# Optimization experiments

Hardware: AMD Instinct MI355X
Metric: run time of the kernel (lower is better)

## Reference

```python
import jax, jax.numpy as jnp
import numpy as np
import math

N_HIDDEN = 256
N_BLOCKS = 15
N_BINARY = 8
NODE_DIM = 16
EDGE_DIM = 4
N_NODES = 20000
N_EDGES = 100000


def setup_inputs() -> dict:
    key = jax.random.key(0)
    ks = iter(jax.random.split(key, 64))

    def lin(i, o):
        return (jax.random.normal(next(ks), (i, o), jnp.float32) / np.sqrt(i)).astype(jnp.float32)

    def lin_s(i, o):  # stacked over N_BLOCKS layers
        return (jax.random.normal(next(ks), (N_BLOCKS, i, o), jnp.float32) / np.sqrt(i)).astype(jnp.float32)

    inp = {
        "x": jax.random.uniform(next(ks), (N_NODES, NODE_DIM), jnp.float32),
        "edge_index": jax.random.randint(next(ks), (2, N_EDGES), 0, N_NODES, jnp.int32),
        "edge_attr": jax.random.uniform(next(ks), (N_EDGES, EDGE_DIM), jnp.float32),
        # conv1: in = NODE_DIM
        "Wq1": lin(NODE_DIM, N_HIDDEN), "bq1": jnp.zeros((N_HIDDEN,), jnp.float32),
        "Wk1": lin(NODE_DIM, N_HIDDEN), "bk1": jnp.zeros((N_HIDDEN,), jnp.float32),
        "Wv1": lin(NODE_DIM, N_HIDDEN), "bv1": jnp.zeros((N_HIDDEN,), jnp.float32),
        "We1": lin(EDGE_DIM, N_HIDDEN),  # lin_edge has no bias in PyG TransformerConv
        "Ws1": lin(NODE_DIM, N_HIDDEN), "bs1": jnp.zeros((N_HIDDEN,), jnp.float32),
        # 15 residual blocks: in = N_HIDDEN, stacked params
        "Wq": lin_s(N_HIDDEN, N_HIDDEN), "bq": jnp.zeros((N_BLOCKS, N_HIDDEN), jnp.float32),
        "Wk": lin_s(N_HIDDEN, N_HIDDEN), "bk": jnp.zeros((N_BLOCKS, N_HIDDEN), jnp.float32),
        "Wv": lin_s(N_HIDDEN, N_HIDDEN), "bv": jnp.zeros((N_BLOCKS, N_HIDDEN), jnp.float32),
        "We": lin_s(EDGE_DIM, N_HIDDEN),
        "Ws": lin_s(N_HIDDEN, N_HIDDEN), "bs": jnp.zeros((N_BLOCKS, N_HIDDEN), jnp.float32),
        # output head
        "Wl": lin(N_HIDDEN, N_BINARY), "bl": jnp.zeros((N_BINARY,), jnp.float32),
        "scale": jnp.asarray([2.0 ** i for i in range(N_BINARY)], jnp.float32),
    }
    return inp


def _tconv(h, ea_emb_src_params, src, dst, n):
    """PyG TransformerConv (heads=1) with edge features."""
    wq, bq, wk, bk, wv, bv, we, ws, bs, ea = ea_emb_src_params
    q = h @ wq + bq          # [N, C]
    k = h @ wk + bk
    v = h @ wv + bv
    e = ea @ we              # [E, C] edge embedding
    ke = k[src] + e          # [E, C]
    alpha = jnp.sum(q[dst] * ke, axis=-1) / math.sqrt(N_HIDDEN)  # [E]
    m = jax.ops.segment_max(alpha, dst, num_segments=n)
    a = jnp.exp(alpha - m[dst])
    s = jax.ops.segment_sum(a, dst, num_segments=n)
    attn = a / (s[dst] + 1e-16)
    out = jax.ops.segment_sum(attn[:, None] * (v[src] + e), dst, num_segments=n)
    return out + h @ ws + bs  # root_weight skip


def reference(x, edge_index, edge_attr,
              Wq1, bq1, Wk1, bk1, Wv1, bv1, We1, Ws1, bs1,
              Wq, bq, Wk, bk, Wv, bv, We, Ws, bs,
              Wl, bl, scale):
    n = x.shape[0]
    src, dst = edge_index[0], edge_index[1]
    h = jnp.log(x + 1.0)
    ea = jnp.log(edge_attr + 1.0)
    h = _tconv(h, (Wq1, bq1, Wk1, bk1, Wv1, bv1, We1, Ws1, bs1, ea), src, dst, n)

    def block(carry, p):
        wq, bq_, wk, bk_, wv, bv_, we, ws, bs_ = p
        std = jax.lax.stop_gradient(jnp.std(carry, axis=-1, ddof=1, keepdims=True))
        h2 = jax.nn.relu(carry / std)
        y = _tconv(h2, (wq, bq_, wk, bk_, wv, bv_, we, ws, bs_, ea), src, dst, n)
        return carry + y, None

    h, _ = jax.lax.scan(block, h, (Wq, bq, Wk, bk, Wv, bv, We, Ws, bs))
    h = h / math.sqrt(N_BLOCKS)
    h = h @ Wl + bl
    return jnp.sum(h * scale, axis=-1, keepdims=True)
```

## Files before the change

kernel.cpp:

```cpp
#include <hip/hip_runtime.h>
#include <math.h>

typedef short bf16x8 __attribute__((ext_vector_type(8)));
typedef float f32x4 __attribute__((ext_vector_type(4)));
typedef _Float16 h16x8 __attribute__((ext_vector_type(8)));
typedef _Float16 h16x4 __attribute__((ext_vector_type(4)));
typedef _Float16 h16x2 __attribute__((ext_vector_type(2)));

static __device__ __forceinline__ float wred_sum(float v){
  #pragma unroll
  for (int o = 32; o > 0; o >>= 1) v += __shfl_xor(v, o, 64);
  return v;
}

static __device__ __forceinline__ unsigned short f2bf(float x){
  union { float f; unsigned int u; } c; c.f = x;
  unsigned int u = c.u;
  return (unsigned short)((u + 0x7FFFu + ((u >> 16) & 1u)) >> 16);
}

__global__ void prep_kernel(const float* __restrict__ x, const float* __restrict__ ea_in,
                            float* __restrict__ hx, float* __restrict__ ea,
                            int nx, int ne){
  int i = blockIdx.x * 256 + threadIdx.x;
  if (i < nx) hx[i] = logf(x[i] + 1.f);
  if (i < ne) ea[i] = logf(ea_in[i] + 1.f);
}

__global__ void zero_kernel(int* __restrict__ c, int n){
  int i = blockIdx.x * 256 + threadIdx.x;
  if (i < n) c[i] = 0;
}

__global__ void hist_kernel(const int* __restrict__ dst, int* __restrict__ counts, int E){
  int i = blockIdx.x * 256 + threadIdx.x;
  if (i < E) atomicAdd(&counts[dst[i]], 1);
}

__global__ __launch_bounds__(1024) void scan_kernel(const int* __restrict__ counts,
                                                    int* __restrict__ row_ptr,
                                                    int* __restrict__ cursor, int N){
  __shared__ int woff[16];
  __shared__ int carry_s;
  int t = threadIdx.x, lane = t & 63, wid = t >> 6;
  if (t == 0) carry_s = 0;
  __syncthreads();
  for (int base = 0; base < N; base += 1024){
    int i = base + t;
    int v = (i < N) ? counts[i] : 0;
    int incl = v;
    #pragma unroll
    for (int o = 1; o < 64; o <<= 1){
      int tmp = __shfl_up(incl, o, 64);
      if (lane >= o) incl += tmp;
    }
    if (lane == 63) woff[wid] = incl;
    __syncthreads();
    if (t < 16){
      int w = woff[t];
      int inc2 = w;
      #pragma unroll
      for (int o = 1; o < 16; o <<= 1){
        int tmp = __shfl_up(inc2, o, 16);
        if (t >= o) inc2 += tmp;
      }
      woff[t] = inc2 - w;
    }
    __syncthreads();
    int ex = carry_s + woff[wid] + incl - v;
    if (i < N){ row_ptr[i] = ex; cursor[i] = ex; }
    __syncthreads();
    if (t == 1023) carry_s = ex + v;
    __syncthreads();
  }
  if (t == 0) row_ptr[N] = carry_s;
}

__global__ void scatter_kernel(const int* __restrict__ src, const int* __restrict__ dst,
                               const float* __restrict__ ea,
                               int* __restrict__ cursor,
                               int* __restrict__ src_csr, float* __restrict__ ea_csr, int E){
  int i = blockIdx.x * 256 + threadIdx.x;
  if (i < E){
    int p = atomicAdd(&cursor[dst[i]], 1);
    src_csr[p] = src[i];
    *(float4*)&ea_csr[(size_t)p * 4] = *(const float4*)&ea[(size_t)i * 4];
  }
}

__global__ void wlscale_kernel(const float* __restrict__ Wl, const float* __restrict__ bl,
                               const float* __restrict__ scale, float* __restrict__ wlsc){
  int c = threadIdx.x;
  float s = 0.f;
  #pragma unroll
  for (int j = 0; j < 8; j++) s += Wl[c * 8 + j] * scale[j];
  wlsc[c] = s;
  if (c == 0){
    float b = 0.f;
    #pragma unroll
    for (int j = 0; j < 8; j++) b += bl[j] * scale[j];
    wlsc[256] = b;
  }
}

__global__ __launch_bounds__(256) void pack_w_kernel(
    const float* __restrict__ Wq, const float* __restrict__ Wk,
    const float* __restrict__ Wv, const float* __restrict__ Ws,
    unsigned short* __restrict__ Wp)
{
  __shared__ float t[32][33];
  int l   = blockIdx.z;
  int k0  = blockIdx.x * 32;
  int n0g = blockIdx.y * 32;
  int w   = n0g >> 8;
  int n0  = n0g & 255;
  const float* W = ((w == 0) ? Wq : (w == 1) ? Wk : (w == 2) ? Wv : Ws) + (size_t)l * 65536;
  int rr = threadIdx.x >> 3;
  int cc = (threadIdx.x & 7) * 4;
  float4 vv = *(const float4*)&W[(size_t)(k0 + rr) * 256 + n0 + cc];
  t[rr][cc + 0] = vv.x; t[rr][cc + 1] = vv.y; t[rr][cc + 2] = vv.z; t[rr][cc + 3] = vv.w;
  __syncthreads();
  ushort4 o;
  o.x = f2bf(t[cc + 0][rr]);
  o.y = f2bf(t[cc + 1][rr]);
  o.z = f2bf(t[cc + 2][rr]);
  o.w = f2bf(t[cc + 3][rr]);
  *(ushort4*)&Wp[(size_t)l * 262144 + (size_t)(n0g + rr) * 256 + k0 + cc] = o;
}

__global__ void pack_b_kernel(const float* __restrict__ bq, const float* __restrict__ bk,
                              const float* __restrict__ bv, const float* __restrict__ bs,
                              float* __restrict__ bp){
  int i = blockIdx.x * 256 + threadIdx.x;
  if (i < 15 * 256){
    int l = i >> 8, n = i & 255;
    bp[l * 1024 + 0   + n] = bq[i];
    bp[l * 1024 + 256 + n] = bk[i];
    bp[l * 1024 + 512 + n] = bv[i];
    bp[l * 1024 + 768 + n] = bs[i];
  }
}

__global__ __launch_bounds__(256) void pack_wqe_kernel(
    const float* __restrict__ Wq, const float* __restrict__ We,
    const float* __restrict__ bq, float* __restrict__ Wqe, float* __restrict__ bqe)
{
  __shared__ float We_s[1024];
  int l = blockIdx.x;
  for (int i = threadIdx.x; i < 1024; i += 256) We_s[i] = We[(size_t)l * 1024 + i];
  __syncthreads();
  int k = threadIdx.x;
  const float* wrow = Wq + (size_t)l * 65536 + (size_t)k * 256;
  float s0 = 0.f, s1 = 0.f, s2 = 0.f, s3 = 0.f;
  for (int c = 0; c < 256; c++){
    float wv = wrow[c];
    s0 += wv * We_s[c];
    s1 += wv * We_s[256 + c];
    s2 += wv * We_s[512 + c];
    s3 += wv * We_s[768 + c];
  }
  float4 o; o.x = s0; o.y = s1; o.z = s2; o.w = s3;
  *(float4*)&Wqe[((size_t)l * 256 + k) * 4] = o;
  if (k < 4){
    float b = 0.f;
    for (int c = 0; c < 256; c++) b += bq[l * 256 + c] * We_s[k * 256 + c];
    bqe[l * 4 + k] = b;
  }
}

__global__ __launch_bounds__(256) void qwe1_kernel(const _Float16* __restrict__ qkvh,
                                                   const float* __restrict__ We1,
                                                   float* __restrict__ qwe, int N){
  __shared__ float We_s[1024];
  for (int i = threadIdx.x; i < 1024; i += 256) We_s[i] = We1[i];
  __syncthreads();
  int wid = threadIdx.x >> 6, lane = threadIdx.x & 63;
  int n = blockIdx.x * 4 + wid;
  if (n >= N) return;
  int c0 = lane * 4;
  h16x4 qr = *(const h16x4*)&qkvh[(size_t)n * 768 + c0];
  float q0 = (float)qr[0], q1 = (float)qr[1], q2 = (float)qr[2], q3 = (float)qr[3];
  float4 o;
  #pragma unroll
  for (int j = 0; j < 4; j++){
    float s = q0 * We_s[j * 256 + c0] + q1 * We_s[j * 256 + c0 + 1]
            + q2 * We_s[j * 256 + c0 + 2] + q3 * We_s[j * 256 + c0 + 3];
    s = wred_sum(s);
    if (j == 0) o.x = s; else if (j == 1) o.y = s; else if (j == 2) o.z = s; else o.w = s;
  }
  if (lane == 0) *(float4*)&qwe[(size_t)n * 4] = o;
}

__global__ __launch_bounds__(256) void gemm1_kernel(
    const float* __restrict__ A,
    const float* __restrict__ W0, const float* __restrict__ W1,
    const float* __restrict__ W2, const float* __restrict__ W3,
    const float* __restrict__ B0, const float* __restrict__ B1,
    const float* __restrict__ B2, const float* __restrict__ B3,
    _Float16* __restrict__ qkvh, _Float16* __restrict__ slh, int N)
{
  __shared__ float As[64][16];
  int nb = blockIdx.x * 64;
  {
    int row = nb + (threadIdx.x >> 2);
    int qq = (threadIdx.x & 3) * 4;
    float4 a = make_float4(0.f, 0.f, 0.f, 0.f);
    if (row < N) a = *(const float4*)&A[row * 16 + qq];
    *(float4*)&As[threadIdx.x >> 2][qq] = a;
  }
  __syncthreads();
  int col = threadIdx.x;
  #pragma unroll
  for (int w = 0; w < 4; w++){
    const float* W  = (w == 0) ? W0 : (w == 1) ? W1 : (w == 2) ? W2 : W3;
    const float* Bi = (w == 0) ? B0 : (w == 1) ? B1 : (w == 2) ? B2 : B3;
    float wr[16];
    #pragma unroll
    for (int kk = 0; kk < 16; kk++) wr[kk] = W[kk * 256 + col];
    float bias = Bi[col];
    for (int r = 0; r < 64; r++){
      int row = nb + r;
      if (row >= N) break;
      float acc = bias;
      #pragma unroll
      for (int kk = 0; kk < 16; kk++) acc += As[r][kk] * wr[kk];
      if (w < 3) qkvh[(size_t)row * 768 + w * 256 + col] = (_Float16)acc;
      else       slh[(size_t)row * 256 + col] = (_Float16)acc;
    }
  }
}

__global__ __launch_bounds__(256, 3) void gemm_mfma_kernel(
    const unsigned short* __restrict__ A,
    const unsigned short* __restrict__ Wp,
    const float* __restrict__ bp,
    _Float16* __restrict__ qkvh,
    _Float16* __restrict__ slh,
    int M)
{
  __shared__ unsigned short lds[2 * 128 * 64];
  unsigned short* ldsA = lds;
  unsigned short* ldsB = lds + 128 * 64;
  const int tid  = threadIdx.x;
  const int wave = tid >> 6, lane = tid & 63;
  const int wm = wave >> 1, wn = wave & 1;
  const int rt  = (int)gridDim.x;
  const int lin = (int)blockIdx.x + rt * (int)blockIdx.y;
  const int gt  = (lin & 7) * rt + (lin >> 3);
  const int m0 = (gt >> 3) * 128;
  const int n0 = (gt & 7) * 128;

  f32x4 acc[4][4] = {};

  const int srow  = lane >> 3;
  const int sc16  = lane & 7;
  const int skgrp = sc16 ^ (srow & 7);

  for (int k0 = 0; k0 < 256; k0 += 64){
    #pragma unroll
    for (int it = 0; it < 4; ++it){
      int lrow = wave * 32 + it * 8;
      const unsigned short* gA = A + (size_t)(m0 + lrow + srow) * 256 + k0 + skgrp * 8;
      __builtin_amdgcn_global_load_lds((const __attribute__((address_space(1))) unsigned int*)gA,
          (__attribute__((address_space(3))) unsigned int*)(ldsA + lrow * 64), 16, 0, 0);
      const unsigned short* gB = Wp + (size_t)(n0 + lrow + srow) * 256 + k0 + skgrp * 8;
      __builtin_amdgcn_global_load_lds((const __attribute__((address_space(1))) unsigned int*)gB,
          (__attribute__((address_space(3))) unsigned int*)(ldsB + lrow * 64), 16, 0, 0);
    }
    __syncthreads();

    bf16x8 af[4][2], bfr[4][2];
    #pragma unroll
    for (int mb = 0; mb < 4; ++mb){
      int r = wm * 64 + mb * 16 + (lane & 15);
      #pragma unroll
      for (int ks = 0; ks < 2; ++ks){
        int kg = ks * 4 + (lane >> 4);
        af[mb][ks] = *(const bf16x8*)&ldsA[r * 64 + ((kg ^ (r & 7)) * 8)];
      }
    }
    #pragma unroll
    for (int nb = 0; nb < 4; ++nb){
      int r = wn * 64 + nb * 16 + (lane & 15);
      #pragma unroll
      for (int ks = 0; ks < 2; ++ks){
        int kg = ks * 4 + (lane >> 4);
        bfr[nb][ks] = *(const bf16x8*)&ldsB[r * 64 + ((kg ^ (r & 7)) * 8)];
      }
    }
    #pragma unroll
    for (int mb = 0; mb < 4; ++mb){
      #pragma unroll
      for (int nb = 0; nb < 4; ++nb){
        acc[mb][nb] = __builtin_amdgcn_mfma_f32_16x16x32_bf16(af[mb][0], bfr[nb][0], acc[mb][nb], 0, 0, 0);
        acc[mb][nb] = __builtin_amdgcn_mfma_f32_16x16x32_bf16(af[mb][1], bfr[nb][1], acc[mb][nb], 0, 0, 0);
      }
    }
    __syncthreads();
  }

  #pragma unroll
  for (int nb = 0; nb < 4; ++nb){
    int col = n0 + wn * 64 + nb * 16 + (lane & 15);
    float bias = bp[col];
    #pragma unroll
    for (int mb = 0; mb < 4; ++mb){
      #pragma unroll
      for (int r4 = 0; r4 < 4; ++r4){
        int row = m0 + wm * 64 + mb * 16 + (lane >> 4) * 4 + r4;
        if (row < M){
          float o = acc[mb][nb][r4] + bias;
          if (col < 768) qkvh[(size_t)row * 768 + col] = (_Float16)o;
          else           slh[(size_t)row * 256 + (col - 768)] = (_Float16)o;
        }
      }
    }
  }
}

__global__ __launch_bounds__(256) void agg_kernel(
    const _Float16* __restrict__ qkvh,
    const _Float16* __restrict__ slh,
    const float* __restrict__ qwe,
    const float* __restrict__ ea_csr,
    const int* __restrict__ src_csr,
    const float* __restrict__ We,
    const float* __restrict__ Wqe_next,
    const float* __restrict__ bqe_next,
    const int* __restrict__ row_ptr,
    const float* __restrict__ h_in, float* __restrict__ h_out,
    unsigned short* __restrict__ h2b, float* __restrict__ qwe_out,
    const float* __restrict__ wlsc, float* __restrict__ out,
    int RESID, int LAST, int N)
{
  int wid = threadIdx.x >> 6, lane = threadIdx.x & 63;
  int n = blockIdx.x * 4 + wid;
  if (n >= N) return;
  int c0 = lane * 4;
  int glane = lane >> 3;
  int slane = lane & 7;

  float4 qwe4 = *(const float4*)&qwe[(size_t)n * 4];
  const _Float16* qrow = qkvh + (size_t)n * 768 + slane * 32;
  union hu { h16x8 v; h16x2 p[4]; };
  hu qf[4];
  #pragma unroll
  for (int u = 0; u < 4; ++u) qf[u].v = *(const h16x8*)(qrow + u * 8);

  float m = -INFINITY, ssum = 0.f;
  float a0 = 0.f, a1 = 0.f, a2 = 0.f, a3 = 0.f;
  float ec0 = 0.f, ec1 = 0.f, ec2 = 0.f, ec3 = 0.f;
  int e0 = row_ptr[n], e1 = row_ptr[n + 1];

  for (int base = e0; base < e1; base += 8){
    int cnt = min(8, e1 - base);
    int eg = base + ((glane < cnt) ? glane : (cnt - 1));
    int sg = src_csr[eg];
    float4 eag = *(const float4*)&ea_csr[(size_t)eg * 4];
    const _Float16* krow = qkvh + (size_t)sg * 768 + 256 + slane * 32;
    float dot = 0.f;
    #pragma unroll
    for (int u = 0; u < 4; ++u){
      hu kf;
      kf.v = *(const h16x8*)(krow + u * 8);
      #pragma unroll
      for (int pp = 0; pp < 4; ++pp){
#if __has_builtin(__builtin_amdgcn_fdot2)
        dot = __builtin_amdgcn_fdot2(qf[u].p[pp], kf.p[pp], dot, false);
#else
        dot += (float)qf[u].p[pp][0] * (float)kf.p[pp][0] + (float)qf[u].p[pp][1] * (float)kf.p[pp][1];
#endif
      }
    }
    #pragma unroll
    for (int o = 1; o < 8; o <<= 1) dot += __shfl_xor(dot, o, 64);
    float alpha_g = (dot + qwe4.x * eag.x + qwe4.y * eag.y + qwe4.z * eag.z + qwe4.w * eag.w) * 0.0625f;
    float aj[8];
    #pragma unroll
    for (int j = 0; j < 8; ++j){
      aj[j] = __shfl(alpha_g, j << 3, 64);
      if (j >= cnt) aj[j] = -INFINITY;
    }
    float mc = fmaxf(fmaxf(fmaxf(aj[0], aj[1]), fmaxf(aj[2], aj[3])),
                     fmaxf(fmaxf(aj[4], aj[5]), fmaxf(aj[6], aj[7])));
    float mn = fmaxf(m, mc);
    float corr = expf(m - mn);
    float wj[8];
    float wtot = 0.f;
    #pragma unroll
    for (int j = 0; j < 8; ++j){
      wj[j] = (j < cnt) ? expf(aj[j] - mn) : 0.f;
      wtot += wj[j];
    }
    ssum = ssum * corr + wtot;
    a0 *= corr; a1 *= corr; a2 *= corr; a3 *= corr;
    ec0 *= corr; ec1 *= corr; ec2 *= corr; ec3 *= corr;
    m = mn;
    #pragma unroll
    for (int j = 0; j < 8; ++j){
      if (j < cnt){
        int sj = __shfl(sg, j << 3, 64);
        h16x4 vr = *(const h16x4*)&qkvh[(size_t)sj * 768 + 512 + c0];
        float4 er = *(const float4*)&ea_csr[(size_t)(base + j) * 4];
        a0 += wj[j] * (float)vr[0];
        a1 += wj[j] * (float)vr[1];
        a2 += wj[j] * (float)vr[2];
        a3 += wj[j] * (float)vr[3];
        ec0 += wj[j] * er.x;
        ec1 += wj[j] * er.y;
        ec2 += wj[j] * er.z;
        ec3 += wj[j] * er.w;
      }
    }
  }

  float inv = 1.f / (ssum + 1e-16f);
  float4 W0 = *(const float4*)&We[0 * 256 + c0];
  float4 W1 = *(const float4*)&We[1 * 256 + c0];
  float4 W2 = *(const float4*)&We[2 * 256 + c0];
  float4 W3 = *(const float4*)&We[3 * 256 + c0];
  float emb0 = ec0 * W0.x + ec1 * W1.x + ec2 * W2.x + ec3 * W3.x;
  float emb1 = ec0 * W0.y + ec1 * W1.y + ec2 * W2.y + ec3 * W3.y;
  float emb2 = ec0 * W0.z + ec1 * W1.z + ec2 * W2.z + ec3 * W3.z;
  float emb3 = ec0 * W0.w + ec1 * W1.w + ec2 * W2.w + ec3 * W3.w;
  h16x4 slv4 = *(const h16x4*)&slh[(size_t)n * 256 + c0];
  float y0 = (a0 + emb0) * inv + (float)slv4[0];
  float y1 = (a1 + emb1) * inv + (float)slv4[1];
  float y2 = (a2 + emb2) * inv + (float)slv4[2];
  float y3 = (a3 + emb3) * inv + (float)slv4[3];
  float o0, o1, o2, o3;
  if (RESID){
    float4 hp = *(const float4*)&h_in[(size_t)n * 256 + c0];
    o0 = hp.x + y0; o1 = hp.y + y1; o2 = hp.z + y2; o3 = hp.w + y3;
  } else {
    o0 = y0; o1 = y1; o2 = y2; o3 = y3;
  }
  if (LAST){
    float4 wv = *(const float4*)&wlsc[c0];
    float pp = o0 * wv.x + o1 * wv.y + o2 * wv.z + o3 * wv.w;
    pp = wred_sum(pp);
    if (lane == 0) out[n] = pp * (1.f / sqrtf(15.f)) + wlsc[256];
    return;
  }
  float4 ho; ho.x = o0; ho.y = o1; ho.z = o2; ho.w = o3;
  *(float4*)&h_out[(size_t)n * 256 + c0] = ho;
  float mean = wred_sum(o0 + o1 + o2 + o3) * (1.f / 256.f);
  float d0 = o0 - mean, d1 = o1 - mean, d2 = o2 - mean, d3 = o3 - mean;
  float var = wred_sum(d0 * d0 + d1 * d1 + d2 * d2 + d3 * d3) * (1.f / 255.f);
  float invstd = 1.f / sqrtf(var);
  float t0 = fmaxf(o0 * invstd, 0.f);
  float t1 = fmaxf(o1 * invstd, 0.f);
  float t2 = fmaxf(o2 * invstd, 0.f);
  float t3 = fmaxf(o3 * invstd, 0.f);
  ushort4 hb;
  hb.x = f2bf(t0); hb.y = f2bf(t1); hb.z = f2bf(t2); hb.w = f2bf(t3);
  *(ushort4*)&h2b[(size_t)n * 256 + c0] = hb;
  if (Wqe_next){
    float4 g0 = *(const float4*)&Wqe_next[(c0 + 0) * 4];
    float4 g1 = *(const float4*)&Wqe_next[(c0 + 1) * 4];
    float4 g2 = *(const float4*)&Wqe_next[(c0 + 2) * 4];
    float4 g3 = *(const float4*)&Wqe_next[(c0 + 3) * 4];
    float s0 = t0 * g0.x + t1 * g1.x + t2 * g2.x + t3 * g3.x;
    float s1 = t0 * g0.y + t1 * g1.y + t2 * g2.y + t3 * g3.y;
    float s2 = t0 * g0.z + t1 * g1.z + t2 * g2.z + t3 * g3.z;
    float s3 = t0 * g0.w + t1 * g1.w + t2 * g2.w + t3 * g3.w;
    s0 = wred_sum(s0); s1 = wred_sum(s1); s2 = wred_sum(s2); s3 = wred_sum(s3);
    if (lane == 0){
      float4 bq4 = *(const float4*)bqe_next;
      float4 o; o.x = s0 + bq4.x; o.y = s1 + bq4.y; o.z = s2 + bq4.z; o.w = s3 + bq4.w;
      *(float4*)&qwe_out[(size_t)n * 4] = o;
    }
  }
}

extern "C" void kernel_launch(void* const* d_in, const int* in_sizes, int n_in,
                              void* d_out, int out_size, void* d_ws, size_t ws_size,
                              hipStream_t stream)
{
  const float* x     = (const float*)d_in[0];
  const int*   eidx  = (const int*)d_in[1];
  const float* Wq1 = (const float*)d_in[3];  const float* bq1 = (const float*)d_in[4];
  const float* Wk1 = (const float*)d_in[5];  const float* bk1 = (const float*)d_in[6];
  const float* Wv1 = (const float*)d_in[7];  const float* bv1 = (const float*)d_in[8];
  const float* We1 = (const float*)d_in[9];
  const float* Ws1 = (const float*)d_in[10]; const float* bs1 = (const float*)d_in[11];
  const float* Wq = (const float*)d_in[12];  const float* bq = (const float*)d_in[13];
  const float* Wk = (const float*)d_in[14];  const float* bk = (const float*)d_in[15];
  const float* Wv = (const float*)d_in[16];  const float* bv = (const float*)d_in[17];
  const float* We = (const float*)d_in[18];
  const float* Ws = (const float*)d_in[19];  const float* bs = (const float*)d_in[20];
  const float* Wl = (const float*)d_in[21];  const float* bl = (const float*)d_in[22];
  const float* scale = (const float*)d_in[23];
  (void)n_in; (void)ws_size;

  int N = in_sizes[0] / 16;
  int E = in_sizes[2] / 4;
  int Mpad = (N + 127) & ~127;
  float* out = (float*)d_out;
  (void)out_size;

  char* p = (char*)d_ws;
  auto alloc = [&](size_t bytes) -> char* {
    char* r = p; p += (bytes + 255) & ~(size_t)255; return r;
  };
  float* hx   = (float*)alloc((size_t)N * 16 * 4);
  float* ea   = (float*)alloc((size_t)E * 4 * 4);
  float* h    = (float*)alloc((size_t)N * 256 * 4);
  unsigned short* h2b = (unsigned short*)alloc((size_t)Mpad * 256 * 2);
  _Float16* qkvh = (_Float16*)alloc((size_t)N * 768 * 2);
  _Float16* slh  = (_Float16*)alloc((size_t)N * 256 * 2);
  float* qwe  = (float*)alloc((size_t)N * 4 * 4);
  float* ea_csr = (float*)alloc((size_t)E * 4 * 4);
  int* src_csr  = (int*)alloc((size_t)E * 4);
  unsigned short* Wp  = (unsigned short*)alloc((size_t)15 * 1024 * 256 * 2);
  float* bp   = (float*)alloc((size_t)15 * 1024 * 4);
  float* Wqe  = (float*)alloc((size_t)15 * 256 * 4 * 4);
  float* bqe  = (float*)alloc((size_t)15 * 4 * 4);
  float* wlsc = (float*)alloc(257 * 4);
  int* counts  = (int*)alloc((size_t)N * 4);
  int* cursor  = (int*)alloc((size_t)N * 4);
  int* row_ptr = (int*)alloc(((size_t)N + 1) * 4);

  const int* srcp = eidx;
  const int* dstp = eidx + E;

  int nx = N * 16, ne = E * 4;
  int big = nx > ne ? nx : ne;

  zero_kernel<<<(N + 255) / 256, 256, 0, stream>>>(counts, N);
  prep_kernel<<<(big + 255) / 256, 256, 0, stream>>>(x, (const float*)d_in[2], hx, ea, nx, ne);
  hist_kernel<<<(E + 255) / 256, 256, 0, stream>>>(dstp, counts, E);
  scan_kernel<<<1, 1024, 0, stream>>>(counts, row_ptr, cursor, N);
  scatter_kernel<<<(E + 255) / 256, 256, 0, stream>>>(srcp, dstp, ea, cursor,
                                                      src_csr, ea_csr, E);
  wlscale_kernel<<<1, 256, 0, stream>>>(Wl, bl, scale, wlsc);
  pack_w_kernel<<<dim3(8, 32, 15), 256, 0, stream>>>(Wq, Wk, Wv, Ws, Wp);
  pack_b_kernel<<<15, 256, 0, stream>>>(bq, bk, bv, bs, bp);
  pack_wqe_kernel<<<15, 256, 0, stream>>>(Wq, We, bq, Wqe, bqe);

  gemm1_kernel<<<(N + 63) / 64, 256, 0, stream>>>(hx, Wq1, Wk1, Wv1, Ws1,
                                                  bq1, bk1, bv1, bs1, qkvh, slh, N);
  qwe1_kernel<<<(N + 3) / 4, 256, 0, stream>>>(qkvh, We1, qwe, N);
  agg_kernel<<<(N + 3) / 4, 256, 0, stream>>>(qkvh, slh, qwe, ea_csr, src_csr, We1,
                                              Wqe, bqe, row_ptr,
                                              h, h, h2b, qwe, wlsc, out, 0, 0, N);

  for (int l = 0; l < 15; l++){
    gemm_mfma_kernel<<<dim3(Mpad / 128, 8), 256, 0, stream>>>(
        h2b, Wp + (size_t)l * 262144, bp + (size_t)l * 1024, qkvh, slh, N);
    int last = (l == 14);
    const float* wqe_n = (l < 14) ? (Wqe + (size_t)(l + 1) * 1024) : nullptr;
    const float* bqe_n = (l < 14) ? (bqe + (size_t)(l + 1) * 4) : nullptr;
    agg_kernel<<<(N + 3) / 4, 256, 0, stream>>>(qkvh, slh, qwe, ea_csr, src_csr,
                                                We + (size_t)l * 1024,
                                                wqe_n, bqe_n, row_ptr,
                                                h, h, h2b, qwe, wlsc, out, 1, last, N);
  }
}
```

Measured before the change: 1.259 ms.

## Stage GEMM epilogue through LDS for coalesced stores; prefetch V gathers in agg

The GEMM epilogue now writes the fp16 accumulator tile into swizzled LDS and then stores 16-byte vectors per thread, replacing scattered 2-byte global stores. In the aggregation kernel, the V-row and edge-attribute gathers for a group of 8 edges are issued before the q·k dot product, so their latency overlaps with the softmax math. The skip and residual loads are also hoisted to the start of the kernel. This raises register pressure in the agg kernel and reuses the GEMM LDS buffer, which assumes it holds at least 128x128 halves.

```diff
diff --git a/kernel.cpp b/kernel.cpp
--- a/kernel.cpp
+++ b/kernel.cpp
@@ -299,20 +299,41 @@
     __syncthreads();
   }
 
+  _Float16* lt = (_Float16*)lds;
   #pragma unroll
   for (int nb = 0; nb < 4; ++nb){
-    int col = n0 + wn * 64 + nb * 16 + (lane & 15);
-    float bias = bp[col];
+    int col = wn * 64 + nb * 16 + (lane & 15);
+    float bias = bp[n0 + col];
     #pragma unroll
     for (int mb = 0; mb < 4; ++mb){
       #pragma unroll
       for (int r4 = 0; r4 < 4; ++r4){
-        int row = m0 + wm * 64 + mb * 16 + (lane >> 4) * 4 + r4;
-        if (row < M){
-          float o = acc[mb][nb][r4] + bias;
-          if (col < 768) qkvh[(size_t)row * 768 + col] = (_Float16)o;
-          else           slh[(size_t)row * 256 + (col - 768)] = (_Float16)o;
-        }
+        int row = wm * 64 + mb * 16 + (lane >> 4) * 4 + r4;
+        lt[row * 128 + (col ^ (((row >> 2) & 3) << 4))] = (_Float16)(acc[mb][nb][r4] + bias);
+      }
+    }
+  }
+  __syncthreads();
+  int tr = tid >> 4;
+  int tc = (tid & 15) * 8;
+  if (n0 < 768){
+    #pragma unroll
+    for (int it = 0; it < 8; ++it){
+      int row = tr + it * 16;
+      int grow = m0 + row;
+      if (grow < M){
+        h16x8 v8 = *(const h16x8*)&lt[row * 128 + (tc ^ (((row >> 2) & 3) << 4))];
+        *(h16x8*)&qkvh[(size_t)grow * 768 + n0 + tc] = v8;
+      }
+    }
+  } else {
+    #pragma unroll
+    for (int it = 0; it < 8; ++it){
+      int row = tr + it * 16;
+      int grow = m0 + row;
+      if (grow < M){
+        h16x8 v8 = *(const h16x8*)&lt[row * 128 + (tc ^ (((row >> 2) & 3) << 4))];
+        *(h16x8*)&slh[(size_t)grow * 256 + (n0 - 768) + tc] = v8;
       }
     }
   }
@@ -340,7 +361,11 @@
   int glane = lane >> 3;
   int slane = lane & 7;
 
+  int e0 = row_ptr[n], e1 = row_ptr[n + 1];
   float4 qwe4 = *(const float4*)&qwe[(size_t)n * 4];
+  h16x4 slv4 = *(const h16x4*)&slh[(size_t)n * 256 + c0];
+  float4 hp = make_float4(0.f, 0.f, 0.f, 0.f);
+  if (RESID) hp = *(const float4*)&h_in[(size_t)n * 256 + c0];
   const _Float16* qrow = qkvh + (size_t)n * 768 + slane * 32;
   union hu { h16x8 v; h16x2 p[4]; };
   hu qf[4];
@@ -350,12 +375,22 @@
   float m = -INFINITY, ssum = 0.f;
   float a0 = 0.f, a1 = 0.f, a2 = 0.f, a3 = 0.f;
   float ec0 = 0.f, ec1 = 0.f, ec2 = 0.f, ec3 = 0.f;
-  int e0 = row_ptr[n], e1 = row_ptr[n + 1];
 
   for (int base = e0; base < e1; base += 8){
     int cnt = min(8, e1 - base);
     int eg = base + ((glane < cnt) ? glane : (cnt - 1));
     int sg = src_csr[eg];
+    int sj[8];
+    #pragma unroll
+    for (int j = 0; j < 8; ++j) sj[j] = __shfl(sg, j << 3, 64);
+    h16x4 vr[8]; float4 er[8];
+    #pragma unroll
+    for (int j = 0; j < 8; ++j){
+      if (j < cnt){
+        vr[j] = *(const h16x4*)&qkvh[(size_t)sj[j] * 768 + 512 + c0];
+        er[j] = *(const float4*)&ea_csr[(size_t)(base + j) * 4];
+      }
+    }
     float4 eag = *(const float4*)&ea_csr[(size_t)eg * 4];
     const _Float16* krow = qkvh + (size_t)sg * 768 + 256 + slane * 32;
     float dot = 0.f;
@@ -399,17 +434,14 @@
     #pragma unroll
     for (int j = 0; j < 8; ++j){
       if (j < cnt){
-        int sj = __shfl(sg, j << 3, 64);
-        h16x4 vr = *(const h16x4*)&qkvh[(size_t)sj * 768 + 512 + c0];
-        float4 er = *(const float4*)&ea_csr[(size_t)(base + j) * 4];
-        a0 += wj[j] * (float)vr[0];
-        a1 += wj[j] * (float)vr[1];
-        a2 += wj[j] * (float)vr[2];
-        a3 += wj[j] * (float)vr[3];
-        ec0 += wj[j] * er.x;
-        ec1 += wj[j] * er.y;
-        ec2 += wj[j] * er.z;
-        ec3 += wj[j] * er.w;
+        a0 += wj[j] * (float)vr[j][0];
+        a1 += wj[j] * (float)vr[j][1];
+        a2 += wj[j] * (float)vr[j][2];
+        a3 += wj[j] * (float)vr[j][3];
+        ec0 += wj[j] * er[j].x;
+        ec1 += wj[j] * er[j].y;
+        ec2 += wj[j] * er[j].z;
+        ec3 += wj[j] * er[j].w;
       }
     }
   }
@@ -423,18 +455,11 @@
   float emb1 = ec0 * W0.y + ec1 * W1.y + ec2 * W2.y + ec3 * W3.y;
   float emb2 = ec0 * W0.z + ec1 * W1.z + ec2 * W2.z + ec3 * W3.z;
   float emb3 = ec0 * W0.w + ec1 * W1.w + ec2 * W2.w + ec3 * W3.w;
-  h16x4 slv4 = *(const h16x4*)&slh[(size_t)n * 256 + c0];
   float y0 = (a0 + emb0) * inv + (float)slv4[0];
   float y1 = (a1 + emb1) * inv + (float)slv4[1];
   float y2 = (a2 + emb2) * inv + (float)slv4[2];
   float y3 = (a3 + emb3) * inv + (float)slv4[3];
-  float o0, o1, o2, o3;
-  if (RESID){
-    float4 hp = *(const float4*)&h_in[(size_t)n * 256 + c0];
-    o0 = hp.x + y0; o1 = hp.y + y1; o2 = hp.z + y2; o3 = hp.w + y3;
-  } else {
-    o0 = y0; o1 = y1; o2 = y2; o3 = y3;
-  }
+  float o0 = hp.x + y0, o1 = hp.y + y1, o2 = hp.z + y2, o3 = hp.w + y3;
   if (LAST){
     float4 wv = *(const float4*)&wlsc[c0];
     float pp = o0 * wv.x + o1 * wv.y + o2 * wv.z + o3 * wv.w;
```

Result: faster. 1.043 ms (-17.1%).
